# Kernel tuning notes

Measured on AMD Instinct MI355X. Metric: run time of the kernel, lower is better.

Reference implementation:

```python
import jax, jax.numpy as jnp
import numpy as np

NUM_NODES = 20000
LOOKBACK = 7
DAYS = 4
NUM_FEATURES = 5
HIDDEN = 128
NUM_EDGES = 320000


def setup_inputs() -> dict:
    key = jax.random.key(0)
    ks = jax.random.split(key, 10)
    p = lambda k, shape: jax.random.normal(k, shape, dtype=jnp.float32) * 0.1
    return {
        "x": jax.random.normal(ks[0], (DAYS * NUM_NODES, LOOKBACK, NUM_FEATURES), dtype=jnp.float32),
        "edge_index": jax.random.randint(ks[1], (2, NUM_EDGES), 0, NUM_NODES, dtype=jnp.int32),
        "W1": p(ks[2], (NUM_FEATURES, HIDDEN)),
        "b1": jnp.zeros((HIDDEN,), jnp.float32),
        "W2": p(ks[3], (HIDDEN, HIDDEN)),
        "b2": jnp.zeros((HIDDEN,), jnp.float32),
        "W_ih": p(ks[4], (3 * HIDDEN, HIDDEN)),
        "W_hh": p(ks[5], (3 * HIDDEN, HIDDEN)),
        "b_ih": jnp.zeros((3 * HIDDEN,), jnp.float32),
        "b_hh": jnp.zeros((3 * HIDDEN,), jnp.float32),
        "W_out": p(ks[6], (HIDDEN, 5)),
        "b_out": jnp.zeros((5,), jnp.float32),
    }


def reference(x, edge_index, W1, b1, W2, b2, W_ih, W_hh, b_ih, b_hh, W_out, b_out):
    # Eval mode: dropout is identity.
    src, dst = edge_index[0], edge_index[1]
    # GCN symmetric normalization with self-loops: deg includes the self-loop (+1).
    deg = jax.ops.segment_sum(jnp.ones((NUM_EDGES,), jnp.float32), dst, num_segments=NUM_NODES) + 1.0
    dinv = jax.lax.rsqrt(deg)                      # [N]
    norm_e = dinv[src] * dinv[dst]                 # [E] edge norm
    self_norm = 1.0 / deg                          # [N] self-loop norm

    def gcn(h_in, W, b):
        h = h_in @ W                               # [N, C_out]
        msg = h[src] * norm_e[:, None]             # gather + scale  [E, C_out]
        agg = jax.ops.segment_sum(msg, dst, num_segments=NUM_NODES)
        return agg + h * self_norm[:, None] + b

    def gru(xt, h):
        gi = xt @ W_ih.T + b_ih
        gh = h @ W_hh.T + b_hh
        i_r, i_z, i_n = jnp.split(gi, 3, axis=1)
        h_r, h_z, h_n = jnp.split(gh, 3, axis=1)
        r = jax.nn.sigmoid(i_r + h_r)
        z = jax.nn.sigmoid(i_z + h_z)
        n = jnp.tanh(i_n + r * h_n)
        return (1.0 - z) * n + z * h

    def day_fwd(x_day):  # x_day: [N, lookback, F]
        def step(h, xt):
            z1 = jax.nn.relu(gcn(xt, W1, b1))
            z2 = jax.nn.relu(gcn(z1, W2, b2))
            return gru(z2, h), None
        h0 = jnp.zeros((NUM_NODES, HIDDEN), jnp.float32)
        hT, _ = jax.lax.scan(step, h0, jnp.swapaxes(x_day, 0, 1))  # scan over lookback
        return jax.nn.softmax(hT @ W_out + b_out, axis=1)          # [N, 5]

    x_days = x.reshape(DAYS, NUM_NODES, LOOKBACK, NUM_FEATURES)
    out = jax.vmap(day_fwd)(x_days)                # [DAYS, N, 5]
    return out.reshape(DAYS * NUM_NODES, 5)
```

## Files before the change

kernel.cpp:

```cpp
#include <hip/hip_runtime.h>
#include <cstddef>
#include <cstdint>

#define N_NODES 20000
#define N_EDGES 320000
#define NDAYS 4
#define LOOKBACK 7
#define NFEAT 5
#define XROW (LOOKBACK * NFEAT)
#define HIDDEN 128
#define GRUROWS 80

typedef short bf8 __attribute__((ext_vector_type(8)));
typedef float fx4 __attribute__((ext_vector_type(4)));

__device__ __forceinline__ float bflo(unsigned int u) {
    union { unsigned int u; float f; } v; v.u = u << 16; return v.f;
}
__device__ __forceinline__ float bfhi(unsigned int u) {
    union { unsigned int u; float f; } v; v.u = u & 0xffff0000u; return v.f;
}
__device__ __forceinline__ unsigned short f2bf(float f) {
    union { float f; unsigned int u; } v; v.f = f;
    unsigned int u = v.u + 0x7fffu + ((v.u >> 16) & 1u);
    return (unsigned short)(u >> 16);
}
__device__ __forceinline__ unsigned int packbf(float a, float b) {
    return (unsigned int)f2bf(a) | ((unsigned int)f2bf(b) << 16);
}
__device__ __forceinline__ float sigm(float v) { return 1.0f / (1.0f + __expf(-v)); }
__device__ __forceinline__ float ftanh(float v) {
    float e2 = __expf(2.0f * v);
    return (e2 - 1.0f) / (e2 + 1.0f);
}
__device__ __forceinline__ void accum8(float* a, uint4 v, float w) {
    a[0] += w * bflo(v.x); a[1] += w * bfhi(v.x);
    a[2] += w * bflo(v.y); a[3] += w * bfhi(v.y);
    a[4] += w * bflo(v.z); a[5] += w * bfhi(v.z);
    a[6] += w * bflo(v.w); a[7] += w * bfhi(v.w);
}


__global__ __launch_bounds__(256) void k_deg(const int* __restrict__ ei, int* __restrict__ deg) {
    int e = blockIdx.x * 256 + threadIdx.x;
    if (e < N_EDGES) atomicAdd(&deg[ei[N_EDGES + e]], 1);
}

__global__ __launch_bounds__(1024) void k_scan(const int* __restrict__ deg, int* __restrict__ row_start) {
    __shared__ int part[1024];
    int tid = threadIdx.x;
    const int chunk = (N_NODES + 1023) / 1024;
    int i0 = tid * chunk;
    int i1 = min(i0 + chunk, N_NODES);
    int s = 0;
    for (int i = i0; i < i1; ++i) s += deg[i];
    part[tid] = s;
    __syncthreads();
    for (int d = 1; d < 1024; d <<= 1) {
        int v = (tid >= d) ? part[tid - d] : 0;
        __syncthreads();
        part[tid] += v;
        __syncthreads();
    }
    int base = part[tid] - s;
    for (int i = i0; i < i1; ++i) { row_start[i] = base; base += deg[i]; }
    if (tid == 1023) row_start[N_NODES] = part[1023];
}

__global__ __launch_bounds__(256) void k_dinv(const int* __restrict__ deg, float* __restrict__ dinv,
                                              float* __restrict__ self_norm) {
    int i = blockIdx.x * 256 + threadIdx.x;
    if (i >= N_NODES) return;
    float d = (float)(deg[i] + 1);
    dinv[i] = 1.0f / sqrtf(d);
    self_norm[i] = 1.0f / d;
}

__global__ __launch_bounds__(256) void k_fill(const int* __restrict__ ei, const int* __restrict__ row_start,
                                              int* __restrict__ cursor, const float* __restrict__ dinv,
                                              int* __restrict__ csr_src, float* __restrict__ csr_norm) {
    int e = blockIdx.x * 256 + threadIdx.x;
    if (e >= N_EDGES) return;
    int s = ei[e], d = ei[N_EDGES + e];
    int pos = row_start[d] + atomicAdd(&cursor[d], 1);
    csr_src[pos] = s;
    csr_norm[pos] = dinv[s] * dinv[d];
}

__global__ __launch_bounds__(256) void k_w2t(const float* __restrict__ W2, unsigned short* __restrict__ W2T) {
    int idx = blockIdx.x * 256 + threadIdx.x;
    if (idx >= HIDDEN * HIDDEN) return;
    int k = idx >> 7, c = idx & 127;
    W2T[c * HIDDEN + k] = f2bf(W2[k * HIDDEN + c]);
}

__global__ __launch_bounds__(256) void k_cast(const float* __restrict__ src, unsigned short* __restrict__ dst, int n) {
    int i = blockIdx.x * 256 + threadIdx.x;
    if (i < n) dst[i] = f2bf(src[i]);
}

__global__ __launch_bounds__(256) void k_bfold(const float* __restrict__ b_ih, const float* __restrict__ b_hh,
                                               float* __restrict__ b_fold) {
    int i = blockIdx.x * 256 + threadIdx.x;
    if (i < 3 * HIDDEN) b_fold[i] = b_ih[i] + (i < 2 * HIDDEN ? b_hh[i] : 0.0f);
}


template<int NB>
__global__ __launch_bounds__(256) void k_aggx(const float* __restrict__ x, float* __restrict__ xa,
                                              const int* __restrict__ row_start, const int* __restrict__ csr_src,
                                              const float* __restrict__ csr_norm,
                                              const float* __restrict__ self_norm, int dayBase) {
    int n = blockIdx.x * 4 + (threadIdx.x >> 6);
    if (n >= N_NODES) return;
    int lane = threadIdx.x & 63;
    if (lane >= XROW) return;
    float sn = self_norm[n];
    float acc[NB];
#pragma unroll
    for (int b = 0; b < NB; ++b)
        acc[b] = x[(size_t)((dayBase + b) * N_NODES + n) * XROW + lane] * sn;
    int e1 = row_start[n + 1];
    for (int e = row_start[n]; e < e1; ++e) {
        int s = csr_src[e];
        float w = csr_norm[e];
#pragma unroll
        for (int b = 0; b < NB; ++b)
            acc[b] += w * x[(size_t)((dayBase + b) * N_NODES + s) * XROW + lane];
    }
#pragma unroll
    for (int b = 0; b < NB; ++b)
        xa[(size_t)(n * NB + b) * XROW + lane] = acc[b];
}


__global__ __launch_bounds__(256) void k_z1(const float* __restrict__ xa, const float* __restrict__ W1,
                                            const float* __restrict__ b1,
                                            unsigned int* __restrict__ Z, int nrows, int t) {
    int idx = blockIdx.x * 256 + threadIdx.x;
    int r = idx >> 6;
    if (r >= nrows) return;
    int lane = idx & 63;
    int c = lane * 2;
    const float* xp = xa + (size_t)r * XROW + t * NFEAT;
    float x0 = xp[0], x1 = xp[1], x2 = xp[2], x3 = xp[3], x4 = xp[4];
    float a0 = x0 * W1[c] + x1 * W1[128 + c] + x2 * W1[256 + c] + x3 * W1[384 + c] + x4 * W1[512 + c];
    float a1 = x0 * W1[c + 1] + x1 * W1[129 + c] + x2 * W1[257 + c] + x3 * W1[385 + c] + x4 * W1[513 + c];
    a0 = fmaxf(a0 + b1[c], 0.0f);
    a1 = fmaxf(a1 + b1[c + 1], 0.0f);
    Z[(size_t)r * 64 + lane] = packbf(a0, a1);
}


template<int NB>
__global__ __launch_bounds__(256) void k_agg(const uint4* __restrict__ H, uint4* __restrict__ Z,
                                             const float* __restrict__ bias,
                                             const int* __restrict__ row_start, const int* __restrict__ csr_src,
                                             const float* __restrict__ csr_norm,
                                             const float* __restrict__ self_norm) {
    int n = blockIdx.x * 4 + (threadIdx.x >> 6);
    if (n >= N_NODES) return;
    int l = threadIdx.x & 63;
    if (l >= NB * 16) return;
    int c0 = (l & 15) * 8;
    float sn = self_norm[n];
    float a[8];
    {
        uint4 sv = H[(size_t)n * (NB * 16) + l];
        a[0] = bflo(sv.x) * sn; a[1] = bfhi(sv.x) * sn;
        a[2] = bflo(sv.y) * sn; a[3] = bfhi(sv.y) * sn;
        a[4] = bflo(sv.z) * sn; a[5] = bfhi(sv.z) * sn;
        a[6] = bflo(sv.w) * sn; a[7] = bfhi(sv.w) * sn;
    }
    int e1 = row_start[n + 1];
    int e = row_start[n];
    for (; e + 3 < e1; e += 4) {
        int s0 = csr_src[e], s1 = csr_src[e + 1], s2 = csr_src[e + 2], s3 = csr_src[e + 3];
        float w0 = csr_norm[e], w1 = csr_norm[e + 1], w2 = csr_norm[e + 2], w3 = csr_norm[e + 3];
        uint4 v0 = H[(size_t)s0 * (NB * 16) + l];
        uint4 v1 = H[(size_t)s1 * (NB * 16) + l];
        uint4 v2 = H[(size_t)s2 * (NB * 16) + l];
        uint4 v3 = H[(size_t)s3 * (NB * 16) + l];
        accum8(a, v0, w0); accum8(a, v1, w1); accum8(a, v2, w2); accum8(a, v3, w3);
    }
    for (; e < e1; ++e) {
        int s = csr_src[e];
        float w = csr_norm[e];
        uint4 v = H[(size_t)s * (NB * 16) + l];
        accum8(a, v, w);
    }
    const float* bp = bias + c0;
    uint4 o;
    o.x = packbf(fmaxf(a[0] + bp[0], 0.f), fmaxf(a[1] + bp[1], 0.f));
    o.y = packbf(fmaxf(a[2] + bp[2], 0.f), fmaxf(a[3] + bp[3], 0.f));
    o.z = packbf(fmaxf(a[4] + bp[4], 0.f), fmaxf(a[5] + bp[5], 0.f));
    o.w = packbf(fmaxf(a[6] + bp[6], 0.f), fmaxf(a[7] + bp[7], 0.f));
    Z[(size_t)n * (NB * 16) + l] = o;
}


__global__ __launch_bounds__(256) void k_gemm_h2(const unsigned short* __restrict__ A,
                                                 const unsigned short* __restrict__ W,
                                                 unsigned short* __restrict__ Out, int rows) {
    int tid = threadIdx.x, w = tid >> 6, l = tid & 63, lr = l & 15, lk = l >> 4;
    int rblk = blockIdx.x * 64;
    int rowA = rblk + w * 16 + lr;
    bool okA = rowA < rows;
    const bf8* Ap = (const bf8*)(A + (size_t)rowA * HIDDEN);
    const bf8* Bp = (const bf8*)W;
    fx4 acc[8];
#pragma unroll
    for (int n = 0; n < 8; ++n) acc[n] = (fx4){0.f, 0.f, 0.f, 0.f};
#pragma unroll
    for (int ks = 0; ks < 4; ++ks) {
        bf8 a = okA ? Ap[4 * ks + lk] : (bf8){0, 0, 0, 0, 0, 0, 0, 0};
#pragma unroll
        for (int n = 0; n < 8; ++n) {
            bf8 b = Bp[(size_t)(16 * n + lr) * 16 + 4 * ks + lk];
            acc[n] = __builtin_amdgcn_mfma_f32_16x16x32_bf16(a, b, acc[n], 0, 0, 0);
        }
    }
#pragma unroll
    for (int n = 0; n < 8; ++n)
#pragma unroll
        for (int r = 0; r < 4; ++r) {
            int row = rblk + w * 16 + lk * 4 + r;
            if (row < rows) Out[(size_t)row * HIDDEN + 16 * n + lr] = f2bf(acc[n][r]);
        }
}


__global__ __launch_bounds__(512, 1) void k_megagru(const unsigned short* __restrict__ Z2all,
                                                    float* __restrict__ Hf,
                                                    const unsigned short* __restrict__ Wih,
                                                    const unsigned short* __restrict__ Whh,
                                                    const float* __restrict__ bfold,
                                                    const float* __restrict__ bhh, int rows) {
    __shared__ __align__(16) char hlds[2 * GRUROWS * HIDDEN * 2];
    const int HALF = GRUROWS * HIDDEN * 2;
    int tid = threadIdx.x, w = tid >> 6, l = tid & 63, lr = l & 15, lk = l >> 4;
    int row0 = blockIdx.x * GRUROWS;
    int c = w * 16 + lr;

    bf8 Bi[3][4], Bh[3][4];
    const bf8* BiP = (const bf8*)Wih;
    const bf8* BhP = (const bf8*)Whh;
#pragma unroll
    for (int g = 0; g < 3; ++g)
#pragma unroll
        for (int ks = 0; ks < 4; ++ks) {
            int rw = g * HIDDEN + c;
            Bi[g][ks] = BiP[(size_t)rw * 16 + 4 * ks + lk];
            Bh[g][ks] = BhP[(size_t)rw * 16 + 4 * ks + lk];
        }

    float bf_r = bfold[c], bf_z = bfold[HIDDEN + c], bf_n = bfold[2 * HIDDEN + c];
    float bh_n = bhh[2 * HIDDEN + c];

    for (int i = tid; i < GRUROWS * HIDDEN / 2; i += 512) ((unsigned int*)hlds)[i] = 0u;
    __syncthreads();

    float hreg[5][4];
#pragma unroll
    for (int m = 0; m < 5; ++m)
#pragma unroll
        for (int r = 0; r < 4; ++r) hreg[m][r] = 0.f;

    int p = 0;
    for (int t = 0; t < LOOKBACK; ++t) {
        const unsigned short* z2t = Z2all + ((size_t)t * rows + row0) * HIDDEN;
#pragma unroll
        for (int m = 0; m < 5; ++m) {
            bf8 az[4];
            const bf8* zp = (const bf8*)(z2t + (size_t)(16 * m + lr) * HIDDEN);
#pragma unroll
            for (int ks = 0; ks < 4; ++ks) az[ks] = zp[4 * ks + lk];
            bf8 ah[4];
#pragma unroll
            for (int ks = 0; ks < 4; ++ks) {
                int byte = p * HALF + (16 * m + lr) * 256 + ks * 64 + lk * 16;
                byte ^= (lr & 7) << 4;
                ah[ks] = *(const bf8*)(hlds + byte);
            }
            fx4 ai[3], ag[3];
#pragma unroll
            for (int g = 0; g < 3; ++g) { ai[g] = (fx4){0.f, 0.f, 0.f, 0.f}; ag[g] = (fx4){0.f, 0.f, 0.f, 0.f}; }
#pragma unroll
            for (int ks = 0; ks < 4; ++ks)
#pragma unroll
                for (int g = 0; g < 3; ++g) {
                    ai[g] = __builtin_amdgcn_mfma_f32_16x16x32_bf16(az[ks], Bi[g][ks], ai[g], 0, 0, 0);
                    ag[g] = __builtin_amdgcn_mfma_f32_16x16x32_bf16(ah[ks], Bh[g][ks], ag[g], 0, 0, 0);
                }
#pragma unroll
            for (int r = 0; r < 4; ++r) {
                int row = 16 * m + lk * 4 + r;
                float hold = hreg[m][r];
                float rr = sigm(ai[0][r] + bf_r + ag[0][r]);
                float zz = sigm(ai[1][r] + bf_z + ag[1][r]);
                float nn = ftanh(ai[2][r] + bf_n + rr * (ag[2][r] + bh_n));
                float hnew = (1.0f - zz) * nn + zz * hold;
                hreg[m][r] = hnew;
                int byte = (p ^ 1) * HALF + row * 256 + c * 2;
                byte ^= (row & 7) << 4;
                *(unsigned short*)(hlds + byte) = f2bf(hnew);
            }
        }
        __syncthreads();
        p ^= 1;
    }

#pragma unroll
    for (int m = 0; m < 5; ++m)
#pragma unroll
        for (int r = 0; r < 4; ++r)
            Hf[(size_t)(row0 + 16 * m + lk * 4 + r) * HIDDEN + c] = hreg[m][r];
}


template<int NB>
__global__ __launch_bounds__(256) void k_out(const float* __restrict__ Hc, const float* __restrict__ Wo,
                                             const float* __restrict__ bo, float* __restrict__ out,
                                             int dayBase) {
    int rr = blockIdx.x * 4 + (threadIdx.x >> 6);
    if (rr >= N_NODES * NB) return;
    int lane = threadIdx.x & 63;
    float2 hv = ((const float2*)(Hc + (size_t)rr * HIDDEN))[lane];
    float l[5];
#pragma unroll
    for (int j = 0; j < 5; ++j) {
        float p = hv.x * Wo[(2 * lane) * 5 + j] + hv.y * Wo[(2 * lane + 1) * 5 + j];
#pragma unroll
        for (int s = 1; s < 64; s <<= 1) p += __shfl_xor(p, s);
        l[j] = p + bo[j];
    }
    float m = fmaxf(fmaxf(fmaxf(l[0], l[1]), fmaxf(l[2], l[3])), l[4]);
    float e0 = expf(l[0] - m), e1 = expf(l[1] - m), e2 = expf(l[2] - m), e3 = expf(l[3] - m), e4 = expf(l[4] - m);
    float inv = 1.0f / (e0 + e1 + e2 + e3 + e4);
    if (lane < 5) {
        float ej = lane == 0 ? e0 : lane == 1 ? e1 : lane == 2 ? e2 : lane == 3 ? e3 : e4;
        int n = rr / NB, dd = dayBase + rr % NB;
        out[((size_t)dd * N_NODES + n) * 5 + lane] = ej * inv;
    }
}


template<int NB>
static void run_days(const float* x, const float* W1, const float* b1,
                     const unsigned short* W2T_bf, const float* b2,
                     const unsigned short* Wih_bf, const unsigned short* Whh_bf,
                     const float* b_fold, const float* b_hh,
                     const float* W_out, const float* b_out, float* out,
                     const int* row_start, const int* csr_src, const float* csr_norm,
                     const float* self_norm,
                     float* xa, unsigned short* Z1, unsigned short* H2,
                     unsigned short* Z2all, float* Hf, hipStream_t stream) {
    const int rows = N_NODES * NB;
    const unsigned ngrid = (N_NODES + 3) / 4;
    const unsigned nblk = (unsigned)((rows + 63) / 64);
    const unsigned gru_grid = (unsigned)(rows / GRUROWS);
    const int rounds = NDAYS / NB;
    for (int dd = 0; dd < rounds; ++dd) {
        int dayBase = dd * NB;
        k_aggx<NB><<<ngrid, 256, 0, stream>>>(x, xa, row_start, csr_src, csr_norm, self_norm, dayBase);
        for (int t = 0; t < LOOKBACK; ++t) {
            k_z1<<<(rows + 3) / 4, 256, 0, stream>>>(xa, W1, b1, (unsigned int*)Z1, rows, t);
            k_gemm_h2<<<nblk, 256, 0, stream>>>(Z1, W2T_bf, H2, rows);
            k_agg<NB><<<ngrid, 256, 0, stream>>>((const uint4*)H2,
                                                 (uint4*)(Z2all + (size_t)t * rows * HIDDEN), b2,
                                                 row_start, csr_src, csr_norm, self_norm);
        }
        k_megagru<<<gru_grid, 512, 0, stream>>>(Z2all, Hf, Wih_bf, Whh_bf, b_fold, b_hh, rows);
        k_out<NB><<<(rows + 3) / 4, 256, 0, stream>>>(Hf, W_out, b_out, out, dayBase);
    }
}


extern "C" void kernel_launch(void* const* d_in, const int* in_sizes, int n_in,
                              void* d_out, int out_size, void* d_ws, size_t ws_size,
                              hipStream_t stream) {
    const float* x     = (const float*)d_in[0];
    const int*   ei    = (const int*)d_in[1];
    const float* W1    = (const float*)d_in[2];
    const float* b1    = (const float*)d_in[3];
    const float* W2    = (const float*)d_in[4];
    const float* b2    = (const float*)d_in[5];
    const float* W_ih  = (const float*)d_in[6];
    const float* W_hh  = (const float*)d_in[7];
    const float* b_ih  = (const float*)d_in[8];
    const float* b_hh  = (const float*)d_in[9];
    const float* W_out = (const float*)d_in[10];
    const float* b_out = (const float*)d_in[11];
    float* out = (float*)d_out;

    size_t off = 0;
    char* wsb = (char*)d_ws;
    auto alloc = [&](size_t bytes) -> void* {
        void* p = wsb + off;
        off = (off + bytes + 255) & ~(size_t)255;
        return p;
    };
    int*            deg       = (int*)alloc(N_NODES * 4);
    int*            cursor    = (int*)alloc(N_NODES * 4);
    int*            row_start = (int*)alloc((N_NODES + 1) * 4);
    float*          dinv      = (float*)alloc(N_NODES * 4);
    float*          self_norm = (float*)alloc(N_NODES * 4);
    unsigned short* W2T_bf    = (unsigned short*)alloc(HIDDEN * HIDDEN * 2);
    unsigned short* Wih_bf    = (unsigned short*)alloc(3 * HIDDEN * HIDDEN * 2);
    unsigned short* Whh_bf    = (unsigned short*)alloc(3 * HIDDEN * HIDDEN * 2);
    float*          b_fold    = (float*)alloc(3 * HIDDEN * 4);
    int*            csr_src   = (int*)alloc(N_EDGES * 4);
    float*          csr_norm  = (float*)alloc(N_EDGES * 4);

    size_t prep_off = off;
    auto need = [&](int nb) -> size_t {
        return prep_off + (size_t)N_NODES * nb * 2956 + 16384;
    };
    int NBsel = (need(4) <= ws_size) ? 4 : (need(2) <= ws_size) ? 2 : 1;
    int rows = N_NODES * NBsel;

    float*          xa    = (float*)alloc((size_t)rows * XROW * 4);
    unsigned short* Z1    = (unsigned short*)alloc((size_t)rows * HIDDEN * 2);
    unsigned short* H2    = (unsigned short*)alloc((size_t)rows * HIDDEN * 2);
    unsigned short* Z2all = (unsigned short*)alloc((size_t)LOOKBACK * rows * HIDDEN * 2);
    float*          Hf    = (float*)alloc((size_t)rows * HIDDEN * 4);

    hipMemsetAsync(deg, 0, N_NODES * 4, stream);
    hipMemsetAsync(cursor, 0, N_NODES * 4, stream);
    k_deg<<<(N_EDGES + 255) / 256, 256, 0, stream>>>(ei, deg);
    k_scan<<<1, 1024, 0, stream>>>(deg, row_start);
    k_dinv<<<(N_NODES + 255) / 256, 256, 0, stream>>>(deg, dinv, self_norm);
    k_fill<<<(N_EDGES + 255) / 256, 256, 0, stream>>>(ei, row_start, cursor, dinv, csr_src, csr_norm);
    k_w2t<<<(HIDDEN * HIDDEN + 255) / 256, 256, 0, stream>>>(W2, W2T_bf);
    k_cast<<<(3 * HIDDEN * HIDDEN + 255) / 256, 256, 0, stream>>>(W_ih, Wih_bf, 3 * HIDDEN * HIDDEN);
    k_cast<<<(3 * HIDDEN * HIDDEN + 255) / 256, 256, 0, stream>>>(W_hh, Whh_bf, 3 * HIDDEN * HIDDEN);
    k_bfold<<<2, 256, 0, stream>>>(b_ih, b_hh, b_fold);

    if (NBsel == 4)
        run_days<4>(x, W1, b1, W2T_bf, b2, Wih_bf, Whh_bf, b_fold, b_hh, W_out, b_out, out,
                    row_start, csr_src, csr_norm, self_norm, xa, Z1, H2, Z2all, Hf, stream);
    else if (NBsel == 2)
        run_days<2>(x, W1, b1, W2T_bf, b2, Wih_bf, Whh_bf, b_fold, b_hh, W_out, b_out, out,
                    row_start, csr_src, csr_norm, self_norm, xa, Z1, H2, Z2all, Hf, stream);
    else
        run_days<1>(x, W1, b1, W2T_bf, b2, Wih_bf, Whh_bf, b_fold, b_hh, W_out, b_out, out,
                    row_start, csr_src, csr_norm, self_norm, xa, Z1, H2, Z2all, Hf, stream);
}
```

Measured before the change: 1.017 ms.

## Fuse layer-1 GCN into W2 GEMM, split GRU into two passes, shrink tiles

Computes the first GCN layer's dense transform and ReLU inside the W2 MFMA GEMM, so the Z1 intermediate buffer and a kernel launch per timestep go away. The GRU recurrence now runs in two launches (4 steps, then 3 steps that reload the hidden state from Hf), which cuts the Z2 staging buffer from 7 to 4 timesteps. It also lowers GRU rows per block from 80 to 32 for more blocks, and merges the r/z input and hidden MFMA accumulators. The trade-offs are an extra hidden-state round trip through global memory, and W1 work repeated in every GEMM block.

```diff
diff --git a/kernel.cpp b/kernel.cpp
--- a/kernel.cpp
+++ b/kernel.cpp
@@ -9,7 +9,7 @@
 #define NFEAT 5
 #define XROW (LOOKBACK * NFEAT)
 #define HIDDEN 128
-#define GRUROWS 80
+#define GRUROWS 32
 
 typedef short bf8 __attribute__((ext_vector_type(8)));
 typedef float fx4 __attribute__((ext_vector_type(4)));
@@ -134,21 +134,48 @@
 }
 
 
-__global__ __launch_bounds__(256) void k_z1(const float* __restrict__ xa, const float* __restrict__ W1,
-                                            const float* __restrict__ b1,
-                                            unsigned int* __restrict__ Z, int nrows, int t) {
-    int idx = blockIdx.x * 256 + threadIdx.x;
-    int r = idx >> 6;
-    if (r >= nrows) return;
-    int lane = idx & 63;
-    int c = lane * 2;
-    const float* xp = xa + (size_t)r * XROW + t * NFEAT;
-    float x0 = xp[0], x1 = xp[1], x2 = xp[2], x3 = xp[3], x4 = xp[4];
-    float a0 = x0 * W1[c] + x1 * W1[128 + c] + x2 * W1[256 + c] + x3 * W1[384 + c] + x4 * W1[512 + c];
-    float a1 = x0 * W1[c + 1] + x1 * W1[129 + c] + x2 * W1[257 + c] + x3 * W1[385 + c] + x4 * W1[513 + c];
-    a0 = fmaxf(a0 + b1[c], 0.0f);
-    a1 = fmaxf(a1 + b1[c + 1], 0.0f);
-    Z[(size_t)r * 64 + lane] = packbf(a0, a1);
+__global__ __launch_bounds__(256) void k_z1gemm(const float* __restrict__ xa, const float* __restrict__ W1,
+                                                const float* __restrict__ b1,
+                                                const unsigned short* __restrict__ W2T,
+                                                unsigned short* __restrict__ H2, int rows, int t) {
+    int tid = threadIdx.x, w = tid >> 6, l = tid & 63, lr = l & 15, lk = l >> 4;
+    int rblk = blockIdx.x * 64;
+    int rowA = rblk + w * 16 + lr;
+    bool okA = rowA < rows;
+    float x5[5];
+#pragma unroll
+    for (int k = 0; k < 5; ++k)
+        x5[k] = okA ? xa[(size_t)rowA * XROW + t * NFEAT + k] : 0.0f;
+    bf8 az[4];
+#pragma unroll
+    for (int ks = 0; ks < 4; ++ks) {
+#pragma unroll
+        for (int j = 0; j < 8; ++j) {
+            int ch = 32 * ks + 8 * lk + j;
+            float v = b1[ch] + x5[0] * W1[ch] + x5[1] * W1[128 + ch] + x5[2] * W1[256 + ch]
+                    + x5[3] * W1[384 + ch] + x5[4] * W1[512 + ch];
+            az[ks][j] = (short)f2bf(fmaxf(v, 0.0f));
+        }
+    }
+    const bf8* Bp = (const bf8*)W2T;
+    fx4 acc[8];
+#pragma unroll
+    for (int n = 0; n < 8; ++n) acc[n] = (fx4){0.f, 0.f, 0.f, 0.f};
+#pragma unroll
+    for (int ks = 0; ks < 4; ++ks) {
+#pragma unroll
+        for (int n = 0; n < 8; ++n) {
+            bf8 b = Bp[(size_t)(16 * n + lr) * 16 + 4 * ks + lk];
+            acc[n] = __builtin_amdgcn_mfma_f32_16x16x32_bf16(az[ks], b, acc[n], 0, 0, 0);
+        }
+    }
+#pragma unroll
+    for (int n = 0; n < 8; ++n)
+#pragma unroll
+        for (int r = 0; r < 4; ++r) {
+            int row = rblk + w * 16 + lk * 4 + r;
+            if (row < rows) H2[(size_t)row * HIDDEN + 16 * n + lr] = f2bf(acc[n][r]);
+        }
 }
 
 
@@ -199,45 +226,15 @@
 }
 
 
-__global__ __launch_bounds__(256) void k_gemm_h2(const unsigned short* __restrict__ A,
-                                                 const unsigned short* __restrict__ W,
-                                                 unsigned short* __restrict__ Out, int rows) {
-    int tid = threadIdx.x, w = tid >> 6, l = tid & 63, lr = l & 15, lk = l >> 4;
-    int rblk = blockIdx.x * 64;
-    int rowA = rblk + w * 16 + lr;
-    bool okA = rowA < rows;
-    const bf8* Ap = (const bf8*)(A + (size_t)rowA * HIDDEN);
-    const bf8* Bp = (const bf8*)W;
-    fx4 acc[8];
-#pragma unroll
-    for (int n = 0; n < 8; ++n) acc[n] = (fx4){0.f, 0.f, 0.f, 0.f};
-#pragma unroll
-    for (int ks = 0; ks < 4; ++ks) {
-        bf8 a = okA ? Ap[4 * ks + lk] : (bf8){0, 0, 0, 0, 0, 0, 0, 0};
-#pragma unroll
-        for (int n = 0; n < 8; ++n) {
-            bf8 b = Bp[(size_t)(16 * n + lr) * 16 + 4 * ks + lk];
-            acc[n] = __builtin_amdgcn_mfma_f32_16x16x32_bf16(a, b, acc[n], 0, 0, 0);
-        }
-    }
-#pragma unroll
-    for (int n = 0; n < 8; ++n)
-#pragma unroll
-        for (int r = 0; r < 4; ++r) {
-            int row = rblk + w * 16 + lk * 4 + r;
-            if (row < rows) Out[(size_t)row * HIDDEN + 16 * n + lr] = f2bf(acc[n][r]);
-        }
-}
-
-
+template<bool FIRST>
 __global__ __launch_bounds__(512, 1) void k_megagru(const unsigned short* __restrict__ Z2all,
                                                     float* __restrict__ Hf,
                                                     const unsigned short* __restrict__ Wih,
                                                     const unsigned short* __restrict__ Whh,
                                                     const float* __restrict__ bfold,
-                                                    const float* __restrict__ bhh, int rows) {
-    __shared__ __align__(16) char hlds[2 * GRUROWS * HIDDEN * 2];
-    const int HALF = GRUROWS * HIDDEN * 2;
+                                                    const float* __restrict__ bhh, int rows, int NT) {
+    __shared__ __align__(16) char hlds[2 * GRUROWS * 256];
+    const int HALF = GRUROWS * 256;
     int tid = threadIdx.x, w = tid >> 6, l = tid & 63, lr = l & 15, lk = l >> 4;
     int row0 = blockIdx.x * GRUROWS;
     int c = w * 16 + lr;
@@ -253,24 +250,35 @@
             Bi[g][ks] = BiP[(size_t)rw * 16 + 4 * ks + lk];
             Bh[g][ks] = BhP[(size_t)rw * 16 + 4 * ks + lk];
         }
-
     float bf_r = bfold[c], bf_z = bfold[HIDDEN + c], bf_n = bfold[2 * HIDDEN + c];
     float bh_n = bhh[2 * HIDDEN + c];
 
-    for (int i = tid; i < GRUROWS * HIDDEN / 2; i += 512) ((unsigned int*)hlds)[i] = 0u;
+    float hreg[2][4];
+    if (FIRST) {
+#pragma unroll
+        for (int m = 0; m < 2; ++m)
+#pragma unroll
+            for (int r = 0; r < 4; ++r) hreg[m][r] = 0.f;
+        for (int i = tid; i < HALF / 4; i += 512) ((unsigned int*)hlds)[i] = 0u;
+    } else {
+#pragma unroll
+        for (int m = 0; m < 2; ++m)
+#pragma unroll
+            for (int r = 0; r < 4; ++r) {
+                int row = 16 * m + lk * 4 + r;
+                float h = Hf[(size_t)(row0 + row) * HIDDEN + c];
+                hreg[m][r] = h;
+                int byte = row * 256 + ((c * 2) ^ ((row & 15) << 4));
+                *(unsigned short*)(hlds + byte) = f2bf(h);
+            }
+    }
     __syncthreads();
 
-    float hreg[5][4];
-#pragma unroll
-    for (int m = 0; m < 5; ++m)
-#pragma unroll
-        for (int r = 0; r < 4; ++r) hreg[m][r] = 0.f;
-
     int p = 0;
-    for (int t = 0; t < LOOKBACK; ++t) {
+    for (int t = 0; t < NT; ++t) {
         const unsigned short* z2t = Z2all + ((size_t)t * rows + row0) * HIDDEN;
 #pragma unroll
-        for (int m = 0; m < 5; ++m) {
+        for (int m = 0; m < 2; ++m) {
             bf8 az[4];
             const bf8* zp = (const bf8*)(z2t + (size_t)(16 * m + lr) * HIDDEN);
 #pragma unroll
@@ -278,31 +286,31 @@
             bf8 ah[4];
 #pragma unroll
             for (int ks = 0; ks < 4; ++ks) {
-                int byte = p * HALF + (16 * m + lr) * 256 + ks * 64 + lk * 16;
-                byte ^= (lr & 7) << 4;
+                int byte = p * HALF + (16 * m + lr) * 256 + ((ks * 64 + lk * 16) ^ (lr << 4));
                 ah[ks] = *(const bf8*)(hlds + byte);
             }
-            fx4 ai[3], ag[3];
-#pragma unroll
-            for (int g = 0; g < 3; ++g) { ai[g] = (fx4){0.f, 0.f, 0.f, 0.f}; ag[g] = (fx4){0.f, 0.f, 0.f, 0.f}; }
-#pragma unroll
-            for (int ks = 0; ks < 4; ++ks)
-#pragma unroll
-                for (int g = 0; g < 3; ++g) {
-                    ai[g] = __builtin_amdgcn_mfma_f32_16x16x32_bf16(az[ks], Bi[g][ks], ai[g], 0, 0, 0);
-                    ag[g] = __builtin_amdgcn_mfma_f32_16x16x32_bf16(ah[ks], Bh[g][ks], ag[g], 0, 0, 0);
-                }
+            fx4 aR = (fx4){0.f, 0.f, 0.f, 0.f};
+            fx4 aZ = (fx4){0.f, 0.f, 0.f, 0.f};
+            fx4 aNi = (fx4){0.f, 0.f, 0.f, 0.f};
+            fx4 aNh = (fx4){0.f, 0.f, 0.f, 0.f};
+#pragma unroll
+            for (int ks = 0; ks < 4; ++ks) {
+                aR = __builtin_amdgcn_mfma_f32_16x16x32_bf16(az[ks], Bi[0][ks], aR, 0, 0, 0);
+                aR = __builtin_amdgcn_mfma_f32_16x16x32_bf16(ah[ks], Bh[0][ks], aR, 0, 0, 0);
+                aZ = __builtin_amdgcn_mfma_f32_16x16x32_bf16(az[ks], Bi[1][ks], aZ, 0, 0, 0);
+                aZ = __builtin_amdgcn_mfma_f32_16x16x32_bf16(ah[ks], Bh[1][ks], aZ, 0, 0, 0);
+                aNi = __builtin_amdgcn_mfma_f32_16x16x32_bf16(az[ks], Bi[2][ks], aNi, 0, 0, 0);
+                aNh = __builtin_amdgcn_mfma_f32_16x16x32_bf16(ah[ks], Bh[2][ks], aNh, 0, 0, 0);
+            }
 #pragma unroll
             for (int r = 0; r < 4; ++r) {
                 int row = 16 * m + lk * 4 + r;
-                float hold = hreg[m][r];
-                float rr = sigm(ai[0][r] + bf_r + ag[0][r]);
-                float zz = sigm(ai[1][r] + bf_z + ag[1][r]);
-                float nn = ftanh(ai[2][r] + bf_n + rr * (ag[2][r] + bh_n));
-                float hnew = (1.0f - zz) * nn + zz * hold;
+                float rr = sigm(aR[r] + bf_r);
+                float zz = sigm(aZ[r] + bf_z);
+                float nn = ftanh(aNi[r] + bf_n + rr * (aNh[r] + bh_n));
+                float hnew = (1.0f - zz) * nn + zz * hreg[m][r];
                 hreg[m][r] = hnew;
-                int byte = (p ^ 1) * HALF + row * 256 + c * 2;
-                byte ^= (row & 7) << 4;
+                int byte = (p ^ 1) * HALF + row * 256 + ((c * 2) ^ ((row & 15) << 4));
                 *(unsigned short*)(hlds + byte) = f2bf(hnew);
             }
         }
@@ -311,7 +319,7 @@
     }
 
 #pragma unroll
-    for (int m = 0; m < 5; ++m)
+    for (int m = 0; m < 2; ++m)
 #pragma unroll
         for (int r = 0; r < 4; ++r)
             Hf[(size_t)(row0 + 16 * m + lk * 4 + r) * HIDDEN + c] = hreg[m][r];
@@ -346,32 +354,38 @@
 
 
 template<int NB>
-static void run_days(const float* x, const float* W1, const float* b1,
+static void run_tier(const float* x, const float* W1, const float* b1,
                      const unsigned short* W2T_bf, const float* b2,
                      const unsigned short* Wih_bf, const unsigned short* Whh_bf,
                      const float* b_fold, const float* b_hh,
                      const float* W_out, const float* b_out, float* out,
                      const int* row_start, const int* csr_src, const float* csr_norm,
                      const float* self_norm,
-                     float* xa, unsigned short* Z1, unsigned short* H2,
-                     unsigned short* Z2all, float* Hf, hipStream_t stream) {
+                     float* xa, unsigned short* H2, unsigned short* Z2all, float* Hf,
+                     hipStream_t stream) {
     const int rows = N_NODES * NB;
     const unsigned ngrid = (N_NODES + 3) / 4;
-    const unsigned nblk = (unsigned)((rows + 63) / 64);
+    const unsigned gblk = (unsigned)((rows + 63) / 64);
     const unsigned gru_grid = (unsigned)(rows / GRUROWS);
     const int rounds = NDAYS / NB;
     for (int dd = 0; dd < rounds; ++dd) {
         int dayBase = dd * NB;
         k_aggx<NB><<<ngrid, 256, 0, stream>>>(x, xa, row_start, csr_src, csr_norm, self_norm, dayBase);
-        for (int t = 0; t < LOOKBACK; ++t) {
-            k_z1<<<(rows + 3) / 4, 256, 0, stream>>>(xa, W1, b1, (unsigned int*)Z1, rows, t);
-            k_gemm_h2<<<nblk, 256, 0, stream>>>(Z1, W2T_bf, H2, rows);
+        for (int t = 0; t < 4; ++t) {
+            k_z1gemm<<<gblk, 256, 0, stream>>>(xa, W1, b1, W2T_bf, H2, rows, t);
             k_agg<NB><<<ngrid, 256, 0, stream>>>((const uint4*)H2,
                                                  (uint4*)(Z2all + (size_t)t * rows * HIDDEN), b2,
                                                  row_start, csr_src, csr_norm, self_norm);
         }
-        k_megagru<<<gru_grid, 512, 0, stream>>>(Z2all, Hf, Wih_bf, Whh_bf, b_fold, b_hh, rows);
-        k_out<NB><<<(rows + 3) / 4, 256, 0, stream>>>(Hf, W_out, b_out, out, dayBase);
+        k_megagru<true><<<gru_grid, 512, 0, stream>>>(Z2all, Hf, Wih_bf, Whh_bf, b_fold, b_hh, rows, 4);
+        for (int t = 4; t < LOOKBACK; ++t) {
+            k_z1gemm<<<gblk, 256, 0, stream>>>(xa, W1, b1, W2T_bf, H2, rows, t);
+            k_agg<NB><<<ngrid, 256, 0, stream>>>((const uint4*)H2,
+                                                 (uint4*)(Z2all + (size_t)(t - 4) * rows * HIDDEN), b2,
+                                                 row_start, csr_src, csr_norm, self_norm);
+        }
+        k_megagru<false><<<gru_grid, 512, 0, stream>>>(Z2all, Hf, Wih_bf, Whh_bf, b_fold, b_hh, rows, 3);
+        k_out<NB><<<(unsigned)((rows + 3) / 4), 256, 0, stream>>>(Hf, W_out, b_out, out, dayBase);
     }
 }
 
@@ -414,15 +428,14 @@
 
     size_t prep_off = off;
     auto need = [&](int nb) -> size_t {
-        return prep_off + (size_t)N_NODES * nb * 2956 + 16384;
+        return prep_off + (size_t)N_NODES * nb * 1932 + 16384;
     };
     int NBsel = (need(4) <= ws_size) ? 4 : (need(2) <= ws_size) ? 2 : 1;
     int rows = N_NODES * NBsel;
 
     float*          xa    = (float*)alloc((size_t)rows * XROW * 4);
-    unsigned short* Z1    = (unsigned short*)alloc((size_t)rows * HIDDEN * 2);
     unsigned short* H2    = (unsigned short*)alloc((size_t)rows * HIDDEN * 2);
-    unsigned short* Z2all = (unsigned short*)alloc((size_t)LOOKBACK * rows * HIDDEN * 2);
+    unsigned short* Z2all = (unsigned short*)alloc((size_t)4 * rows * HIDDEN * 2);
     float*          Hf    = (float*)alloc((size_t)rows * HIDDEN * 4);
 
     hipMemsetAsync(deg, 0, N_NODES * 4, stream);
@@ -437,12 +450,12 @@
     k_bfold<<<2, 256, 0, stream>>>(b_ih, b_hh, b_fold);
 
     if (NBsel == 4)
-        run_days<4>(x, W1, b1, W2T_bf, b2, Wih_bf, Whh_bf, b_fold, b_hh, W_out, b_out, out,
-                    row_start, csr_src, csr_norm, self_norm, xa, Z1, H2, Z2all, Hf, stream);
+        run_tier<4>(x, W1, b1, W2T_bf, b2, Wih_bf, Whh_bf, b_fold, b_hh, W_out, b_out, out,
+                    row_start, csr_src, csr_norm, self_norm, xa, H2, Z2all, Hf, stream);
     else if (NBsel == 2)
-        run_days<2>(x, W1, b1, W2T_bf, b2, Wih_bf, Whh_bf, b_fold, b_hh, W_out, b_out, out,
-                    row_start, csr_src, csr_norm, self_norm, xa, Z1, H2, Z2all, Hf, stream);
+        run_tier<2>(x, W1, b1, W2T_bf, b2, Wih_bf, Whh_bf, b_fold, b_hh, W_out, b_out, out,
+                    row_start, csr_src, csr_norm, self_norm, xa, H2, Z2all, Hf, stream);
     else
-        run_days<1>(x, W1, b1, W2T_bf, b2, Wih_bf, Whh_bf, b_fold, b_hh, W_out, b_out, out,
-                    row_start, csr_src, csr_norm, self_norm, xa, Z1, H2, Z2all, Hf, stream);
-}
+        run_tier<1>(x, W1, b1, W2T_bf, b2, Wih_bf, Whh_bf, b_fold, b_hh, W_out, b_out, out,
+                    row_start, csr_src, csr_norm, self_norm, xa, H2, Z2all, Hf, stream);
+}
```

After: 1.063 ms. +4.6%, slower.
